# Optimization experiments

Measured on AMD Instinct MI355X. Metric: run time of the kernel, lower is better.

## Reference

```python
import jax, jax.numpy as jnp
import numpy as np

NUM_HEADS = 8
EPS = 1e-6


def setup_inputs() -> dict:
    key = jax.random.key(0)
    ks = jax.random.split(key, 6)
    B, T, E = 2, 4096, 512
    s = 0.02
    x = jax.random.normal(ks[0], (B, T, E), dtype=jnp.float32)
    Wq = jax.random.normal(ks[1], (E, E), dtype=jnp.float32) * s
    Wk = jax.random.normal(ks[2], (E, E), dtype=jnp.float32) * s
    Wv = jax.random.normal(ks[3], (E, E), dtype=jnp.float32) * s
    Wo = jax.random.normal(ks[4], (E, E), dtype=jnp.float32) * s
    bq = jnp.zeros((E,), jnp.float32)
    bk = jnp.zeros((E,), jnp.float32)
    bv = jnp.zeros((E,), jnp.float32)
    bo = jnp.zeros((E,), jnp.float32)
    return {"x": x, "Wq": Wq, "bq": bq, "Wk": Wk, "bk": bk,
            "Wv": Wv, "bv": bv, "Wo": Wo, "bo": bo}


def _linear(x, W, b):
    # torch nn.Linear: y = x @ W.T + b
    return x @ W.T + b


def _feature_map(x):
    return jax.nn.elu(x) + 1.0


def _linear_attention(x, Wq, bq, Wk, bk, Wv, bv, Wo, bo):
    B, T, E = x.shape
    H = NUM_HEADS
    D = E // H

    def heads(y):  # (B,T,E) -> (T,B,H,D), time-major for scan
        return y.reshape(B, T, H, D).transpose(1, 0, 2, 3)

    q = _feature_map(heads(_linear(x, Wq, bq)))
    k = _feature_map(heads(_linear(x, Wk, bk)))
    v = heads(_linear(x, Wv, bv))

    # Causal linear attention: running KV outer-product state S (B,H,D,D)
    # and running key sum z (B,H,D). Equivalent to the naive
    # cumsum-of-outer-products (B,H,T,D,D) formulation, but O(D^2) state.
    S0 = jnp.zeros((B, H, D, D), x.dtype)
    z0 = jnp.zeros((B, H, D), x.dtype)

    def step(carry, qkv):
        S, z = carry
        qt, kt, vt = qkv  # each (B,H,D)
        S = S + kt[..., :, None] * vt[..., None, :]
        z = z + kt
        num = jnp.einsum('bhd,bhde->bhe', qt, S)
        den = jnp.sum(qt * z, axis=-1) + EPS  # (B,H)
        return (S, z), num / den[..., None]

    _, out = jax.lax.scan(step, (S0, z0), (q, k, v))  # (T,B,H,D)
    out = out.transpose(1, 0, 2, 3).reshape(B, T, E)
    return _linear(out, Wo, bo)


def reference(x, Wq, bq, Wk, bk, Wv, bv, Wo, bo):
    return _linear_attention(x, Wq, bq, Wk, bk, Wv, bv, Wo, bo)
```

## Files before the change

kernel.cpp:

```cpp
#include <hip/hip_runtime.h>
#include <hip/hip_bf16.h>

#define T_SEQ 4096
#define EMB   512
#define NH    8
#define HD    64
#define BATCH 2
#define M_ROWS (BATCH * T_SEQ)
#define NCHUNK 64
#define CS     64
#define BHEADS (BATCH * NH)

using bf16 = __hip_bfloat16;
typedef __attribute__((ext_vector_type(8))) short short8;
typedef __attribute__((ext_vector_type(4))) float floatx4;

__device__ __forceinline__ void bf2f(unsigned u, float& lo, float& hi) {
    lo = __uint_as_float((u & 0xffffu) << 16);
    hi = __uint_as_float(u & 0xffff0000u);
}
__device__ __forceinline__ float bs2f(short s) {
    return __uint_as_float(((unsigned)(unsigned short)s) << 16);
}

__device__ __forceinline__ float load_elem(const bf16* p, size_t i) {
    return __bfloat162float(p[i]);
}
__device__ __forceinline__ float load_elem(const float* p, size_t i) {
    return p[i];
}
__device__ __forceinline__ void store_elem(bf16* p, size_t i, float v) {
    p[i] = __float2bfloat16(v);
}
__device__ __forceinline__ void store_elem(float* p, size_t i, float v) {
    p[i] = v;
}
__device__ __forceinline__ short f2bs(float f) {
    bf16 h = __float2bfloat16(f);
    return *reinterpret_cast<short*>(&h);
}
__device__ __forceinline__ void stage8(const bf16* g, short* l) {
    *reinterpret_cast<short8*>(l) = *reinterpret_cast<const short8*>(g);
}
__device__ __forceinline__ void stage8(const float* g, short* l) {
    float4 a = *reinterpret_cast<const float4*>(g);
    float4 b = *reinterpret_cast<const float4*>(g + 4);
    short8 v;
    v[0] = f2bs(a.x); v[1] = f2bs(a.y); v[2] = f2bs(a.z); v[3] = f2bs(a.w);
    v[4] = f2bs(b.x); v[5] = f2bs(b.y); v[6] = f2bs(b.z); v[7] = f2bs(b.w);
    *reinterpret_cast<short8*>(l) = v;
}
template <typename T> struct ModeOf { static constexpr int v = 0; };
template <> struct ModeOf<float>    { static constexpr int v = 1; };

#define LDSTR 72

__global__ void detect_dtype(const unsigned short* __restrict__ xraw,
                             int* __restrict__ flag)
{
    const int lane = threadIdx.x;
    bool bad = false;
    for (int i = 0; i < 64; ++i) {
        const unsigned u = xraw[(size_t)(lane + i * 64) * 2];
        const float f = __uint_as_float(u << 16);
        if (!(fabsf(f) <= 1e9f)) bad = true;
    }
    const unsigned long long m = __ballot(bad);
    if (lane == 0) *flag = (m != 0ull) ? 1 : 0;
}

template <typename T>
__global__ __launch_bounds__(256) void qkv_mfma(
    const int* __restrict__ flag,
    const T* __restrict__ x,
    const T* __restrict__ Wq, const T* __restrict__ bq,
    const T* __restrict__ Wk, const T* __restrict__ bk,
    const T* __restrict__ Wv, const T* __restrict__ bv,
    bf16* __restrict__ Qf, bf16* __restrict__ Kf, bf16* __restrict__ Vf)
{
    if (*flag != ModeOf<T>::v) return;

    const int mtile = blockIdx.x;
    const int ntile = blockIdx.y;
    const int which = ntile >> 2;
    const T* W    = (which == 0) ? Wq : ((which == 1) ? Wk : Wv);
    const T* bias = (which == 0) ? bq : ((which == 1) ? bk : bv);
    bf16* outp    = (which == 0) ? Qf : ((which == 1) ? Kf : Vf);
    const int nbase = (ntile & 3) * 128;
    const int mbase = mtile * 128;

    __shared__ short As[128 * LDSTR];
    __shared__ short Bs[128 * LDSTR];

    const int tid  = threadIdx.x;
    const int wave = tid >> 6, lane = tid & 63;
    const int wm = wave >> 1, wn = wave & 1;
    const int lm = lane & 15, quad = lane >> 4;

    floatx4 acc[4][4];
    const floatx4 zero = {0.f, 0.f, 0.f, 0.f};
    #pragma unroll
    for (int mt = 0; mt < 4; ++mt)
        #pragma unroll
        for (int nt = 0; nt < 4; ++nt) acc[mt][nt] = zero;

    for (int kt = 0; kt < EMB; kt += 64) {
        #pragma unroll
        for (int i = 0; i < 4; ++i) {
            const int c = tid + i * 256;
            const int row = c >> 3, k8 = (c & 7) * 8;
            stage8(x + (size_t)(mbase + row) * EMB + kt + k8, &As[row * LDSTR + k8]);
            stage8(W + (size_t)(nbase + row) * EMB + kt + k8, &Bs[row * LDSTR + k8]);
        }
        __syncthreads();
        #pragma unroll
        for (int ks = 0; ks < 2; ++ks) {
            short8 af[4], bfr[4];
            #pragma unroll
            for (int mt = 0; mt < 4; ++mt)
                af[mt] = *reinterpret_cast<const short8*>(
                    &As[(wm * 64 + mt * 16 + lm) * LDSTR + ks * 32 + quad * 8]);
            #pragma unroll
            for (int nt = 0; nt < 4; ++nt)
                bfr[nt] = *reinterpret_cast<const short8*>(
                    &Bs[(wn * 64 + nt * 16 + lm) * LDSTR + ks * 32 + quad * 8]);
            #pragma unroll
            for (int mt = 0; mt < 4; ++mt)
                #pragma unroll
                for (int nt = 0; nt < 4; ++nt)
                    acc[mt][nt] = __builtin_amdgcn_mfma_f32_16x16x32_bf16(
                        af[mt], bfr[nt], acc[mt][nt], 0, 0, 0);
        }
        __syncthreads();
    }

    #pragma unroll
    for (int nt = 0; nt < 4; ++nt) {
        const int col = nbase + wn * 64 + nt * 16 + lm;
        const float bv_ = load_elem(bias, col);
        const int h = col >> 6, d = col & 63;
        #pragma unroll
        for (int mt = 0; mt < 4; ++mt)
            #pragma unroll
            for (int r = 0; r < 4; ++r) {
                const int row = mbase + wm * 64 + mt * 16 + quad * 4 + r;
                const int b = row >> 12, t = row & (T_SEQ - 1);
                float v = acc[mt][nt][r] + bv_;
                if (which != 2) v = (v > 0.f) ? (v + 1.f) : __expf(v);
                outp[(((size_t)(b * NH + h)) * T_SEQ + t) * HD + d] = __float2bfloat16(v);
            }
    }
}

__global__ __launch_bounds__(256) void chunk_kv(
    const bf16* __restrict__ Kf, const bf16* __restrict__ Vf,
    float* __restrict__ KV, float* __restrict__ ksum)
{
    const int bh = blockIdx.x >> 6;
    const int c  = blockIdx.x & 63;
    __shared__ short Kt[64 * LDSTR];
    __shared__ short Vt[64 * LDSTR];
    const int tid = threadIdx.x;
    const bf16* kp = Kf + ((size_t)bh * T_SEQ + c * CS) * HD;
    const bf16* vp = Vf + ((size_t)bh * T_SEQ + c * CS) * HD;

    #pragma unroll
    for (int j = 0; j < 2; ++j) {
        const int u = j * 256 + tid;
        const int e0 = u * 8;
        const int s = e0 >> 6, d0 = e0 & 63;
        short8 ku = *reinterpret_cast<const short8*>(kp + e0);
        short8 vu = *reinterpret_cast<const short8*>(vp + e0);
        #pragma unroll
        for (int i = 0; i < 8; ++i) {
            Kt[(d0 + i) * LDSTR + s] = ku[i];
            Vt[(d0 + i) * LDSTR + s] = vu[i];
        }
    }
    __syncthreads();

    const int w = tid >> 6, lane = tid & 63;
    const int lm = lane & 15, quad = lane >> 4;

    floatx4 acc[4];
    const floatx4 zero = {0.f, 0.f, 0.f, 0.f};
    #pragma unroll
    for (int nt = 0; nt < 4; ++nt) acc[nt] = zero;

    #pragma unroll
    for (int ks = 0; ks < 2; ++ks) {
        short8 ak = *reinterpret_cast<const short8*>(
            &Kt[(w * 16 + lm) * LDSTR + ks * 32 + quad * 8]);
        #pragma unroll
        for (int nt = 0; nt < 4; ++nt) {
            short8 bv = *reinterpret_cast<const short8*>(
                &Vt[(nt * 16 + lm) * LDSTR + ks * 32 + quad * 8]);
            acc[nt] = __builtin_amdgcn_mfma_f32_16x16x32_bf16(ak, bv, acc[nt], 0, 0, 0);
        }
    }

    float* kvout = KV + ((size_t)bh * NCHUNK + c) * 4096;
    #pragma unroll
    for (int nt = 0; nt < 4; ++nt)
        #pragma unroll
        for (int r = 0; r < 4; ++r) {
            const int dk = w * 16 + quad * 4 + r;
            const int dv = nt * 16 + lm;
            kvout[dk * 64 + dv] = acc[nt][r];
        }

    if (tid < 64) {
        float s = 0.f;
        #pragma unroll 8
        for (int t = 0; t < 64; ++t) s += bs2f(Kt[tid * LDSTR + t]);
        ksum[((size_t)bh * NCHUNK + c) * 64 + tid] = s;
    }
}

__global__ __launch_bounds__(256) void prefix_kv(
    float* __restrict__ KV, float* __restrict__ ksum)
{
    const int bh   = blockIdx.x >> 4;
    const int part = blockIdx.x & 15;
    const int tid  = threadIdx.x;
    const int e    = part * 256 + tid;
    float* base = KV + (size_t)bh * NCHUNK * 4096 + e;

    float s = 0.f;
    #pragma unroll
    for (int cb = 0; cb < 4; ++cb) {
        float v[16];
        #pragma unroll
        for (int i = 0; i < 16; ++i) v[i] = base[(size_t)(cb * 16 + i) * 4096];
        #pragma unroll
        for (int i = 0; i < 16; ++i) {
            const float tmp = v[i];
            base[(size_t)(cb * 16 + i) * 4096] = s;
            s += tmp;
        }
    }

    if (part == 0 && tid < 64) {
        float* zb = ksum + (size_t)bh * NCHUNK * 64 + tid;
        float z = 0.f;
        #pragma unroll
        for (int cb = 0; cb < 4; ++cb) {
            float v[16];
            #pragma unroll
            for (int i = 0; i < 16; ++i) v[i] = zb[(size_t)(cb * 16 + i) * 64];
            #pragma unroll
            for (int i = 0; i < 16; ++i) {
                const float tmp = v[i];
                zb[(size_t)(cb * 16 + i) * 64] = z;
                z += tmp;
            }
        }
    }
}

__global__ __launch_bounds__(256) void attn_mfma(
    const bf16* __restrict__ Qf, const bf16* __restrict__ Kf,
    const bf16* __restrict__ Vf, const float* __restrict__ KV,
    const float* __restrict__ ksum, bf16* __restrict__ Of)
{
    const int bh = blockIdx.x >> 6;
    const int c  = blockIdx.x & 63;
    const int b  = bh >> 3, h = bh & 7;

    __shared__ short Qs [64 * LDSTR];
    __shared__ short Ksn[64 * LDSTR];
    __shared__ short Vt [64 * LDSTR];
    __shared__ short Ps [64 * LDSTR];
    __shared__ float zprev[64];
    __shared__ float rden[64];

    const int tid = threadIdx.x;
    const int w = tid >> 6, lane = tid & 63;
    const int lm = lane & 15, quad = lane >> 4;
    const size_t coff = ((size_t)bh * T_SEQ + c * CS) * HD;
    const float* Sp = KV + ((size_t)bh * NCHUNK + c) * 4096;

    #pragma unroll
    for (int j = 0; j < 2; ++j) {
        const int u  = j * 256 + tid;
        const int e0 = u * 8;
        const int r = e0 >> 6, cc = e0 & 63;
        *reinterpret_cast<short8*>(&Qs [r * LDSTR + cc]) =
            *reinterpret_cast<const short8*>(Qf + coff + e0);
        *reinterpret_cast<short8*>(&Ksn[r * LDSTR + cc]) =
            *reinterpret_cast<const short8*>(Kf + coff + e0);
        short8 vu = *reinterpret_cast<const short8*>(Vf + coff + e0);
        #pragma unroll
        for (int i = 0; i < 8; ++i) Vt[(cc + i) * LDSTR + r] = vu[i];
    }
    if (tid < 64) zprev[tid] = ksum[((size_t)bh * NCHUNK + c) * 64 + tid];
    __syncthreads();

    floatx4 pacc[4];
    const floatx4 zero = {0.f, 0.f, 0.f, 0.f};
    #pragma unroll
    for (int nt = 0; nt < 4; ++nt) pacc[nt] = zero;
    #pragma unroll
    for (int ks = 0; ks < 2; ++ks) {
        short8 aq = *reinterpret_cast<const short8*>(
            &Qs[(w * 16 + lm) * LDSTR + ks * 32 + quad * 8]);
        #pragma unroll
        for (int nt = 0; nt < 4; ++nt) {
            short8 bk = *reinterpret_cast<const short8*>(
                &Ksn[(nt * 16 + lm) * LDSTR + ks * 32 + quad * 8]);
            pacc[nt] = __builtin_amdgcn_mfma_f32_16x16x32_bf16(aq, bk, pacc[nt], 0, 0, 0);
        }
    }
    #pragma unroll
    for (int nt = 0; nt < 4; ++nt)
        #pragma unroll
        for (int r = 0; r < 4; ++r) {
            const int t = w * 16 + quad * 4 + r;
            const int s = nt * 16 + lm;
            Ps[t * LDSTR + s] = f2bs((s <= t) ? pacc[nt][r] : 0.f);
        }

    floatx4 oacc[4];
    #pragma unroll
    for (int nt = 0; nt < 4; ++nt) oacc[nt] = zero;
    for (int d = 0; d < 64; ++d) {
        float qv[4];
        #pragma unroll
        for (int r = 0; r < 4; ++r)
            qv[r] = bs2f(Qs[(w * 16 + quad * 4 + r) * LDSTR + d]);
        #pragma unroll
        for (int nt = 0; nt < 4; ++nt) {
            const float sv = Sp[d * 64 + nt * 16 + lm];
            #pragma unroll
            for (int r = 0; r < 4; ++r) oacc[nt][r] += qv[r] * sv;
        }
    }
    __syncthreads();

    if (tid < 64) {
        float rs = 0.f;
        #pragma unroll 8
        for (int s = 0; s < 64; ++s) rs += bs2f(Ps[tid * LDSTR + s]);
        float dz = 0.f;
        #pragma unroll 8
        for (int d = 0; d < 64; ++d) dz += bs2f(Qs[tid * LDSTR + d]) * zprev[d];
        rden[tid] = 1.f / (rs + dz + 1e-6f);
    }

    #pragma unroll
    for (int ks = 0; ks < 2; ++ks) {
        short8 ap = *reinterpret_cast<const short8*>(
            &Ps[(w * 16 + lm) * LDSTR + ks * 32 + quad * 8]);
        #pragma unroll
        for (int nt = 0; nt < 4; ++nt) {
            short8 bv = *reinterpret_cast<const short8*>(
                &Vt[(nt * 16 + lm) * LDSTR + ks * 32 + quad * 8]);
            oacc[nt] = __builtin_amdgcn_mfma_f32_16x16x32_bf16(ap, bv, oacc[nt], 0, 0, 0);
        }
    }
    __syncthreads();

    #pragma unroll
    for (int nt = 0; nt < 4; ++nt)
        #pragma unroll
        for (int r = 0; r < 4; ++r) {
            const int t  = w * 16 + quad * 4 + r;
            const int dv = nt * 16 + lm;
            const int tg = c * CS + t;
            Of[((size_t)(b * T_SEQ + tg)) * EMB + h * HD + dv] =
                __float2bfloat16(oacc[nt][r] * rden[t]);
        }
}

template <typename T>
__global__ __launch_bounds__(256) void out_proj_mfma(
    const int* __restrict__ flag,
    const bf16* __restrict__ A, const T* __restrict__ Wo,
    const T* __restrict__ bo, T* __restrict__ out)
{
    if (*flag != ModeOf<T>::v) return;

    const int mbase = blockIdx.x * 128;
    const int nbase = blockIdx.y * 128;

    __shared__ short As[128 * LDSTR];
    __shared__ short Bs[128 * LDSTR];

    const int tid  = threadIdx.x;
    const int wave = tid >> 6, lane = tid & 63;
    const int wm = wave >> 1, wn = wave & 1;
    const int lm = lane & 15, quad = lane >> 4;

    floatx4 acc[4][4];
    const floatx4 zero = {0.f, 0.f, 0.f, 0.f};
    #pragma unroll
    for (int mt = 0; mt < 4; ++mt)
        #pragma unroll
        for (int nt = 0; nt < 4; ++nt) acc[mt][nt] = zero;

    for (int kt = 0; kt < EMB; kt += 64) {
        #pragma unroll
        for (int i = 0; i < 4; ++i) {
            const int c = tid + i * 256;
            const int row = c >> 3, k8 = (c & 7) * 8;
            stage8(A  + (size_t)(mbase + row) * EMB + kt + k8, &As[row * LDSTR + k8]);
            stage8(Wo + (size_t)(nbase + row) * EMB + kt + k8, &Bs[row * LDSTR + k8]);
        }
        __syncthreads();
        #pragma unroll
        for (int ks = 0; ks < 2; ++ks) {
            short8 af[4], bfr[4];
            #pragma unroll
            for (int mt = 0; mt < 4; ++mt)
                af[mt] = *reinterpret_cast<const short8*>(
                    &As[(wm * 64 + mt * 16 + lm) * LDSTR + ks * 32 + quad * 8]);
            #pragma unroll
            for (int nt = 0; nt < 4; ++nt)
                bfr[nt] = *reinterpret_cast<const short8*>(
                    &Bs[(wn * 64 + nt * 16 + lm) * LDSTR + ks * 32 + quad * 8]);
            #pragma unroll
            for (int mt = 0; mt < 4; ++mt)
                #pragma unroll
                for (int nt = 0; nt < 4; ++nt)
                    acc[mt][nt] = __builtin_amdgcn_mfma_f32_16x16x32_bf16(
                        af[mt], bfr[nt], acc[mt][nt], 0, 0, 0);
        }
        __syncthreads();
    }

    #pragma unroll
    for (int nt = 0; nt < 4; ++nt) {
        const int col = nbase + wn * 64 + nt * 16 + lm;
        const float bv_ = load_elem(bo, col);
        #pragma unroll
        for (int mt = 0; mt < 4; ++mt)
            #pragma unroll
            for (int r = 0; r < 4; ++r) {
                const int row = mbase + wm * 64 + mt * 16 + quad * 4 + r;
                store_elem(out, (size_t)row * EMB + col, acc[mt][nt][r] + bv_);
            }
    }
}

extern "C" void kernel_launch(void* const* d_in, const int* in_sizes, int n_in,
                              void* d_out, int out_size, void* d_ws, size_t ws_size,
                              hipStream_t stream)
{
    int*  flag = (int*)d_ws;
    bf16* Qf = (bf16*)((char*)d_ws + 64);
    bf16* Kf = Qf + 4194304;
    bf16* Vf = Kf + 4194304;
    float* KV = (float*)(Vf + 4194304);
    float* ks = KV + 4194304;
    bf16* Of = (bf16*)(ks + 65536);

    detect_dtype<<<1, 64, 0, stream>>>((const unsigned short*)d_in[0], flag);

    qkv_mfma<bf16><<<dim3(64, 12), 256, 0, stream>>>(flag,
        (const bf16*)d_in[0],
        (const bf16*)d_in[1], (const bf16*)d_in[2],
        (const bf16*)d_in[3], (const bf16*)d_in[4],
        (const bf16*)d_in[5], (const bf16*)d_in[6],
        Qf, Kf, Vf);
    qkv_mfma<float><<<dim3(64, 12), 256, 0, stream>>>(flag,
        (const float*)d_in[0],
        (const float*)d_in[1], (const float*)d_in[2],
        (const float*)d_in[3], (const float*)d_in[4],
        (const float*)d_in[5], (const float*)d_in[6],
        Qf, Kf, Vf);

    chunk_kv<<<dim3(BHEADS * NCHUNK), 256, 0, stream>>>(Kf, Vf, KV, ks);
    prefix_kv<<<dim3(BHEADS * 16), 256, 0, stream>>>(KV, ks);
    attn_mfma<<<dim3(BHEADS * NCHUNK), 256, 0, stream>>>(Qf, Kf, Vf, KV, ks, Of);

    out_proj_mfma<bf16><<<dim3(64, 4), 256, 0, stream>>>(flag,
        Of, (const bf16*)d_in[7], (const bf16*)d_in[8], (bf16*)d_out);
    out_proj_mfma<float><<<dim3(64, 4), 256, 0, stream>>>(flag,
        Of, (const float*)d_in[7], (const float*)d_in[8], (float*)d_out);
}
```

Before: 171.8 us.

## Pre-convert inputs to bf16, use direct-to-LDS loads, MFMA for inter-chunk term

Adds a conversion kernel that casts x, all weights and biases to bf16 once, so the QKV and output GEMMs stage tiles with global_load_lds (direct global-to-LDS) into unpadded LDS. The attention kernel now stages the chunk prefix state into LDS as bf16 and computes the Q·S term with MFMA instead of a scalar FP32 loop. The dtype detector is widened to 256 threads. The extra conversion pass adds memory traffic, the unpadded LDS layout may cause bank conflicts, and the prefix state is rounded to bf16, which lowers precision.

```diff
diff --git a/kernel.cpp b/kernel.cpp
--- a/kernel.cpp
+++ b/kernel.cpp
@@ -15,29 +15,21 @@
 typedef __attribute__((ext_vector_type(8))) short short8;
 typedef __attribute__((ext_vector_type(4))) float floatx4;
 
-__device__ __forceinline__ void bf2f(unsigned u, float& lo, float& hi) {
-    lo = __uint_as_float((u & 0xffffu) << 16);
-    hi = __uint_as_float(u & 0xffff0000u);
-}
 __device__ __forceinline__ float bs2f(short s) {
     return __uint_as_float(((unsigned)(unsigned short)s) << 16);
-}
-
-__device__ __forceinline__ float load_elem(const bf16* p, size_t i) {
-    return __bfloat162float(p[i]);
-}
-__device__ __forceinline__ float load_elem(const float* p, size_t i) {
-    return p[i];
-}
-__device__ __forceinline__ void store_elem(bf16* p, size_t i, float v) {
-    p[i] = __float2bfloat16(v);
-}
-__device__ __forceinline__ void store_elem(float* p, size_t i, float v) {
-    p[i] = v;
 }
 __device__ __forceinline__ short f2bs(float f) {
     bf16 h = __float2bfloat16(f);
     return *reinterpret_cast<short*>(&h);
+}
+__device__ __forceinline__ float load_elem(const bf16* p, size_t i) {
+    return __bfloat162float(p[i]);
+}
+__device__ __forceinline__ void store_elem(bf16* p, size_t i, float v) {
+    p[i] = __float2bfloat16(v);
+}
+__device__ __forceinline__ void store_elem(float* p, size_t i, float v) {
+    p[i] = v;
 }
 __device__ __forceinline__ void stage8(const bf16* g, short* l) {
     *reinterpret_cast<short8*>(l) = *reinterpret_cast<const short8*>(g);
@@ -53,49 +45,89 @@
 template <typename T> struct ModeOf { static constexpr int v = 0; };
 template <> struct ModeOf<float>    { static constexpr int v = 1; };
 
+__device__ __forceinline__ void gload_lds16(const short* g, short* l) {
+    __builtin_amdgcn_global_load_lds(
+        (const __attribute__((address_space(1))) void*)g,
+        (__attribute__((address_space(3))) void*)l, 16, 0, 0);
+}
+
 #define LDSTR 72
 
 __global__ void detect_dtype(const unsigned short* __restrict__ xraw,
                              int* __restrict__ flag)
 {
-    const int lane = threadIdx.x;
+    __shared__ int bad_s;
+    const int tid = threadIdx.x;
+    if (tid == 0) bad_s = 0;
+    __syncthreads();
     bool bad = false;
-    for (int i = 0; i < 64; ++i) {
-        const unsigned u = xraw[(size_t)(lane + i * 64) * 2];
-        const float f = __uint_as_float(u << 16);
-        if (!(fabsf(f) <= 1e9f)) bad = true;
-    }
-    const unsigned long long m = __ballot(bad);
-    if (lane == 0) *flag = (m != 0ull) ? 1 : 0;
+    #pragma unroll
+    for (int i = 0; i < 2; ++i) {
+        uint4 u = reinterpret_cast<const uint4*>(xraw)[tid + i * 256];
+        const unsigned w[4] = {u.x, u.y, u.z, u.w};
+        #pragma unroll
+        for (int k = 0; k < 4; ++k) {
+            const float f = __uint_as_float(w[k] << 16);
+            if (!(fabsf(f) <= 1e9f)) bad = true;
+        }
+    }
+    if (bad) atomicOr(&bad_s, 1);
+    __syncthreads();
+    if (tid == 0) *flag = bad_s ? 1 : 0;
 }
 
 template <typename T>
-__global__ __launch_bounds__(256) void qkv_mfma(
+__global__ __launch_bounds__(256) void convert_all(
     const int* __restrict__ flag,
     const T* __restrict__ x,
     const T* __restrict__ Wq, const T* __restrict__ bq,
     const T* __restrict__ Wk, const T* __restrict__ bk,
     const T* __restrict__ Wv, const T* __restrict__ bv,
+    const T* __restrict__ Wo, const T* __restrict__ bo,
+    short* __restrict__ xb, short* __restrict__ Wb, short* __restrict__ bb)
+{
+    if (*flag != ModeOf<T>::v) return;
+    const int c = blockIdx.x * 256 + threadIdx.x;
+    if (c < 524288) {
+        stage8(x + (size_t)c * 8, xb + (size_t)c * 8);
+    } else if (c < 655360) {
+        const int c2 = c - 524288;
+        const int w = c2 >> 15;
+        const int off = (c2 & 32767) * 8;
+        const T* src = (w == 0) ? Wq : (w == 1) ? Wk : (w == 2) ? Wv : Wo;
+        stage8(src + off, Wb + w * 262144 + off);
+    } else {
+        const int c3 = c - 655360;
+        const int bsel = c3 >> 6;
+        const int off = (c3 & 63) * 8;
+        const T* src = (bsel == 0) ? bq : (bsel == 1) ? bk : (bsel == 2) ? bv : bo;
+        stage8(src + off, bb + bsel * 512 + off);
+    }
+}
+
+__global__ __launch_bounds__(256) void qkv_gemm_dl(
+    const short* __restrict__ xb, const short* __restrict__ Wb,
+    const short* __restrict__ bb,
     bf16* __restrict__ Qf, bf16* __restrict__ Kf, bf16* __restrict__ Vf)
 {
-    if (*flag != ModeOf<T>::v) return;
-
     const int mtile = blockIdx.x;
     const int ntile = blockIdx.y;
     const int which = ntile >> 2;
-    const T* W    = (which == 0) ? Wq : ((which == 1) ? Wk : Wv);
-    const T* bias = (which == 0) ? bq : ((which == 1) ? bk : bv);
-    bf16* outp    = (which == 0) ? Qf : ((which == 1) ? Kf : Vf);
+    const short* W = Wb + (size_t)which * 262144;
+    const bf16* bias = (const bf16*)(bb + which * 512);
+    bf16* outp = (which == 0) ? Qf : ((which == 1) ? Kf : Vf);
     const int nbase = (ntile & 3) * 128;
     const int mbase = mtile * 128;
 
-    __shared__ short As[128 * LDSTR];
-    __shared__ short Bs[128 * LDSTR];
+    __shared__ short As[128 * 64];
+    __shared__ short Bs[128 * 64];
 
     const int tid  = threadIdx.x;
     const int wave = tid >> 6, lane = tid & 63;
     const int wm = wave >> 1, wn = wave & 1;
     const int lm = lane & 15, quad = lane >> 4;
+    const int srow = lane >> 3;
+    const int scol = (lane & 7) * 8;
 
     floatx4 acc[4][4];
     const floatx4 zero = {0.f, 0.f, 0.f, 0.f};
@@ -106,11 +138,13 @@
 
     for (int kt = 0; kt < EMB; kt += 64) {
         #pragma unroll
-        for (int i = 0; i < 4; ++i) {
-            const int c = tid + i * 256;
-            const int row = c >> 3, k8 = (c & 7) * 8;
-            stage8(x + (size_t)(mbase + row) * EMB + kt + k8, &As[row * LDSTR + k8]);
-            stage8(W + (size_t)(nbase + row) * EMB + kt + k8, &Bs[row * LDSTR + k8]);
+        for (int j = 0; j < 4; ++j) {
+            const int issue = wave * 4 + j;
+            const int row = issue * 8 + srow;
+            gload_lds16(xb + (size_t)(mbase + row) * EMB + kt + scol,
+                        &As[issue * 512]);
+            gload_lds16(W  + (size_t)(nbase + row) * EMB + kt + scol,
+                        &Bs[issue * 512]);
         }
         __syncthreads();
         #pragma unroll
@@ -119,11 +153,11 @@
             #pragma unroll
             for (int mt = 0; mt < 4; ++mt)
                 af[mt] = *reinterpret_cast<const short8*>(
-                    &As[(wm * 64 + mt * 16 + lm) * LDSTR + ks * 32 + quad * 8]);
+                    &As[(wm * 64 + mt * 16 + lm) * 64 + ks * 32 + quad * 8]);
             #pragma unroll
             for (int nt = 0; nt < 4; ++nt)
                 bfr[nt] = *reinterpret_cast<const short8*>(
-                    &Bs[(wn * 64 + nt * 16 + lm) * LDSTR + ks * 32 + quad * 8]);
+                    &Bs[(wn * 64 + nt * 16 + lm) * 64 + ks * 32 + quad * 8]);
             #pragma unroll
             for (int mt = 0; mt < 4; ++mt)
                 #pragma unroll
@@ -137,7 +171,7 @@
     #pragma unroll
     for (int nt = 0; nt < 4; ++nt) {
         const int col = nbase + wn * 64 + nt * 16 + lm;
-        const float bv_ = load_elem(bias, col);
+        const float bv_ = load_elem(bias, col & 511);
         const int h = col >> 6, d = col & 63;
         #pragma unroll
         for (int mt = 0; mt < 4; ++mt)
@@ -271,6 +305,7 @@
     __shared__ short Ksn[64 * LDSTR];
     __shared__ short Vt [64 * LDSTR];
     __shared__ short Ps [64 * LDSTR];
+    __shared__ short St [64 * LDSTR];
     __shared__ float zprev[64];
     __shared__ float rden[64];
 
@@ -293,24 +328,38 @@
         #pragma unroll
         for (int i = 0; i < 8; ++i) Vt[(cc + i) * LDSTR + r] = vu[i];
     }
+    #pragma unroll
+    for (int j = 0; j < 4; ++j) {
+        const int u = j * 256 + tid;
+        const float4 s4 = reinterpret_cast<const float4*>(Sp)[u];
+        const int d = u >> 4;
+        const int dv0 = (u & 15) * 4;
+        St[(dv0 + 0) * LDSTR + d] = f2bs(s4.x);
+        St[(dv0 + 1) * LDSTR + d] = f2bs(s4.y);
+        St[(dv0 + 2) * LDSTR + d] = f2bs(s4.z);
+        St[(dv0 + 3) * LDSTR + d] = f2bs(s4.w);
+    }
     if (tid < 64) zprev[tid] = ksum[((size_t)bh * NCHUNK + c) * 64 + tid];
     __syncthreads();
 
+    const floatx4 zero = {0.f, 0.f, 0.f, 0.f};
+    short8 aq[2];
+    #pragma unroll
+    for (int ks = 0; ks < 2; ++ks)
+        aq[ks] = *reinterpret_cast<const short8*>(
+            &Qs[(w * 16 + lm) * LDSTR + ks * 32 + quad * 8]);
+
     floatx4 pacc[4];
-    const floatx4 zero = {0.f, 0.f, 0.f, 0.f};
     #pragma unroll
     for (int nt = 0; nt < 4; ++nt) pacc[nt] = zero;
     #pragma unroll
-    for (int ks = 0; ks < 2; ++ks) {
-        short8 aq = *reinterpret_cast<const short8*>(
-            &Qs[(w * 16 + lm) * LDSTR + ks * 32 + quad * 8]);
+    for (int ks = 0; ks < 2; ++ks)
         #pragma unroll
         for (int nt = 0; nt < 4; ++nt) {
             short8 bk = *reinterpret_cast<const short8*>(
                 &Ksn[(nt * 16 + lm) * LDSTR + ks * 32 + quad * 8]);
-            pacc[nt] = __builtin_amdgcn_mfma_f32_16x16x32_bf16(aq, bk, pacc[nt], 0, 0, 0);
-        }
-    }
+            pacc[nt] = __builtin_amdgcn_mfma_f32_16x16x32_bf16(aq[ks], bk, pacc[nt], 0, 0, 0);
+        }
     #pragma unroll
     for (int nt = 0; nt < 4; ++nt)
         #pragma unroll
@@ -323,18 +372,14 @@
     floatx4 oacc[4];
     #pragma unroll
     for (int nt = 0; nt < 4; ++nt) oacc[nt] = zero;
-    for (int d = 0; d < 64; ++d) {
-        float qv[4];
-        #pragma unroll
-        for (int r = 0; r < 4; ++r)
-            qv[r] = bs2f(Qs[(w * 16 + quad * 4 + r) * LDSTR + d]);
+    #pragma unroll
+    for (int ks = 0; ks < 2; ++ks)
         #pragma unroll
         for (int nt = 0; nt < 4; ++nt) {
-            const float sv = Sp[d * 64 + nt * 16 + lm];
-            #pragma unroll
-            for (int r = 0; r < 4; ++r) oacc[nt][r] += qv[r] * sv;
-        }
-    }
+            short8 bs = *reinterpret_cast<const short8*>(
+                &St[(nt * 16 + lm) * LDSTR + ks * 32 + quad * 8]);
+            oacc[nt] = __builtin_amdgcn_mfma_f32_16x16x32_bf16(aq[ks], bs, oacc[nt], 0, 0, 0);
+        }
     __syncthreads();
 
     if (tid < 64) {
@@ -373,23 +418,27 @@
 }
 
 template <typename T>
-__global__ __launch_bounds__(256) void out_proj_mfma(
+__global__ __launch_bounds__(256) void out_proj_dl(
     const int* __restrict__ flag,
-    const bf16* __restrict__ A, const T* __restrict__ Wo,
-    const T* __restrict__ bo, T* __restrict__ out)
+    const short* __restrict__ A, const short* __restrict__ Wb,
+    const short* __restrict__ bb, T* __restrict__ out)
 {
     if (*flag != ModeOf<T>::v) return;
 
     const int mbase = blockIdx.x * 128;
     const int nbase = blockIdx.y * 128;
-
-    __shared__ short As[128 * LDSTR];
-    __shared__ short Bs[128 * LDSTR];
+    const short* W = Wb + (size_t)3 * 262144;
+    const bf16* bias = (const bf16*)(bb + 3 * 512);
+
+    __shared__ short As[128 * 64];
+    __shared__ short Bs[128 * 64];
 
     const int tid  = threadIdx.x;
     const int wave = tid >> 6, lane = tid & 63;
     const int wm = wave >> 1, wn = wave & 1;
     const int lm = lane & 15, quad = lane >> 4;
+    const int srow = lane >> 3;
+    const int scol = (lane & 7) * 8;
 
     floatx4 acc[4][4];
     const floatx4 zero = {0.f, 0.f, 0.f, 0.f};
@@ -400,11 +449,13 @@
 
     for (int kt = 0; kt < EMB; kt += 64) {
         #pragma unroll
-        for (int i = 0; i < 4; ++i) {
-            const int c = tid + i * 256;
-            const int row = c >> 3, k8 = (c & 7) * 8;
-            stage8(A  + (size_t)(mbase + row) * EMB + kt + k8, &As[row * LDSTR + k8]);
-            stage8(Wo + (size_t)(nbase + row) * EMB + kt + k8, &Bs[row * LDSTR + k8]);
+        for (int j = 0; j < 4; ++j) {
+            const int issue = wave * 4 + j;
+            const int row = issue * 8 + srow;
+            gload_lds16(A + (size_t)(mbase + row) * EMB + kt + scol,
+                        &As[issue * 512]);
+            gload_lds16(W + (size_t)(nbase + row) * EMB + kt + scol,
+                        &Bs[issue * 512]);
         }
         __syncthreads();
         #pragma unroll
@@ -413,11 +464,11 @@
             #pragma unroll
             for (int mt = 0; mt < 4; ++mt)
                 af[mt] = *reinterpret_cast<const short8*>(
-                    &As[(wm * 64 + mt * 16 + lm) * LDSTR + ks * 32 + quad * 8]);
+                    &As[(wm * 64 + mt * 16 + lm) * 64 + ks * 32 + quad * 8]);
             #pragma unroll
             for (int nt = 0; nt < 4; ++nt)
                 bfr[nt] = *reinterpret_cast<const short8*>(
-                    &Bs[(wn * 64 + nt * 16 + lm) * LDSTR + ks * 32 + quad * 8]);
+                    &Bs[(wn * 64 + nt * 16 + lm) * 64 + ks * 32 + quad * 8]);
             #pragma unroll
             for (int mt = 0; mt < 4; ++mt)
                 #pragma unroll
@@ -431,7 +482,7 @@
     #pragma unroll
     for (int nt = 0; nt < 4; ++nt) {
         const int col = nbase + wn * 64 + nt * 16 + lm;
-        const float bv_ = load_elem(bo, col);
+        const float bv_ = load_elem(bias, col);
         #pragma unroll
         for (int mt = 0; mt < 4; ++mt)
             #pragma unroll
@@ -451,30 +502,36 @@
     bf16* Kf = Qf + 4194304;
     bf16* Vf = Kf + 4194304;
     float* KV = (float*)(Vf + 4194304);
+    short* xb = (short*)KV;
     float* ks = KV + 4194304;
     bf16* Of = (bf16*)(ks + 65536);
-
-    detect_dtype<<<1, 64, 0, stream>>>((const unsigned short*)d_in[0], flag);
-
-    qkv_mfma<bf16><<<dim3(64, 12), 256, 0, stream>>>(flag,
+    short* Wb = (short*)(Of + 4194304);
+    short* bb = Wb + 1048576;
+
+    detect_dtype<<<1, 256, 0, stream>>>((const unsigned short*)d_in[0], flag);
+
+    convert_all<bf16><<<dim3(2561), 256, 0, stream>>>(flag,
         (const bf16*)d_in[0],
         (const bf16*)d_in[1], (const bf16*)d_in[2],
         (const bf16*)d_in[3], (const bf16*)d_in[4],
         (const bf16*)d_in[5], (const bf16*)d_in[6],
-        Qf, Kf, Vf);
-    qkv_mfma<float><<<dim3(64, 12), 256, 0, stream>>>(flag,
+        (const bf16*)d_in[7], (const bf16*)d_in[8],
+        xb, Wb, bb);
+    convert_all<float><<<dim3(2561), 256, 0, stream>>>(flag,
         (const float*)d_in[0],
         (const float*)d_in[1], (const float*)d_in[2],
         (const float*)d_in[3], (const float*)d_in[4],
         (const float*)d_in[5], (const float*)d_in[6],
-        Qf, Kf, Vf);
-
+        (const float*)d_in[7], (const float*)d_in[8],
+        xb, Wb, bb);
+
+    qkv_gemm_dl<<<dim3(64, 12), 256, 0, stream>>>(xb, Wb, bb, Qf, Kf, Vf);
     chunk_kv<<<dim3(BHEADS * NCHUNK), 256, 0, stream>>>(Kf, Vf, KV, ks);
     prefix_kv<<<dim3(BHEADS * 16), 256, 0, stream>>>(KV, ks);
     attn_mfma<<<dim3(BHEADS * NCHUNK), 256, 0, stream>>>(Qf, Kf, Vf, KV, ks, Of);
 
-    out_proj_mfma<bf16><<<dim3(64, 4), 256, 0, stream>>>(flag,
-        Of, (const bf16*)d_in[7], (const bf16*)d_in[8], (bf16*)d_out);
-    out_proj_mfma<float><<<dim3(64, 4), 256, 0, stream>>>(flag,
-        Of, (const float*)d_in[7], (const float*)d_in[8], (float*)d_out);
-}
+    out_proj_dl<bf16><<<dim3(64, 4), 256, 0, stream>>>(flag,
+        (const short*)Of, Wb, bb, (bf16*)d_out);
+    out_proj_dl<float><<<dim3(64, 4), 256, 0, stream>>>(flag,
+        (const short*)Of, Wb, bb, (float*)d_out);
+}
```

Measured after the change: 167.2 us. -2.7%, faster.
